# Performance work log

Measured on AMD Instinct MI355X. Metric: run time of the kernel, lower is better.

Reference implementation:

```python
import jax, jax.numpy as jnp
import numpy as np

B, P, E = 256, 196, 2048           # batch, num_pixels, encoder_size
H, A, EMB = 2048, 512, 300         # hidden, attention, embedding dims
V_IN, V_OUT = 262, 261             # input vocab (classes+2), output (classes+1)
T = 7                              # max_seq_len + 2


def setup_inputs() -> dict:
    key = jax.random.key(0)
    ks = jax.random.split(key, 20)
    s = 0.02
    return {
        "encoder_feature_out": jax.random.normal(ks[0], (B, P, E), jnp.float32),
        "encoder_out": jax.random.normal(ks[1], (B, E), jnp.float32),
        "annotations_X": jax.random.randint(ks[2], (B, T), 0, V_IN),
        "is_train": 1,
        "emb_W": jax.random.normal(ks[3], (V_IN, EMB), jnp.float32) * s,
        "feat_W": jax.random.normal(ks[4], (H, E), jnp.float32) * s,
        "feat_b": jnp.zeros((H,), jnp.float32),
        "W_ih": jax.random.normal(ks[5], (4 * H, EMB + E), jnp.float32) * s,
        "W_hh": jax.random.normal(ks[6], (4 * H, H), jnp.float32) * s,
        "b_ih": jnp.zeros((4 * H,), jnp.float32),
        "b_hh": jnp.zeros((4 * H,), jnp.float32),
        "enc_att_W": jax.random.normal(ks[7], (A, E), jnp.float32) * s,
        "enc_att_b": jnp.zeros((A,), jnp.float32),
        "dec_att_W": jax.random.normal(ks[8], (A, H), jnp.float32) * s,
        "dec_att_b": jnp.zeros((A,), jnp.float32),
        "full_att_W": jax.random.normal(ks[9], (1, A), jnp.float32) * s,
        "full_att_b": jnp.zeros((1,), jnp.float32),
        "fbeta_W": jax.random.normal(ks[10], (E, H), jnp.float32) * s,
        "fbeta_b": jnp.zeros((E,), jnp.float32),
        "fc_W": jax.random.normal(ks[11], (V_OUT, H), jnp.float32) * s,
        "fc_b": jnp.zeros((V_OUT,), jnp.float32),
    }


def _forward(encoder_feature_out, encoder_out, annotations_X,
             emb_W, feat_W, feat_b, W_ih, W_hh, b_ih, b_hh,
             enc_att_W, enc_att_b, dec_att_W, dec_att_b,
             full_att_W, full_att_b, fbeta_W, fbeta_b, fc_W, fc_b):
    enc = encoder_feature_out                                  # (B,P,E)
    # encoder side of additive attention is constant across steps
    att1 = jnp.einsum('bpe,ae->bpa', enc, enc_att_W) + enc_att_b  # (B,P,A)
    h0 = encoder_out @ feat_W.T + feat_b                       # (B,H)
    c0 = jnp.zeros_like(h0)

    def step(carry, ann_t):
        h, c = carry
        # additive attention
        att2 = h @ dec_att_W.T + dec_att_b                     # (B,A)
        e = jax.nn.relu(att1 + att2[:, None, :]) @ full_att_W[0] + full_att_b[0]  # (B,P)
        alpha = jax.nn.softmax(e, axis=1)                      # (B,P)
        awe = jnp.einsum('bp,bpe->be', alpha, enc)             # (B,E)
        gate = jax.nn.sigmoid(h @ fbeta_W.T + fbeta_b)         # (B,E)
        awe = gate * awe
        # LSTMCell (dropout layers in eval mode -> identity)
        x = jnp.concatenate([emb_W[ann_t], awe], axis=1)       # (B,EMB+E)
        gates = x @ W_ih.T + b_ih + h @ W_hh.T + b_hh          # (B,4H)
        i, f, g, o = jnp.split(gates, 4, axis=1)
        c = jax.nn.sigmoid(f) * c + jax.nn.sigmoid(i) * jnp.tanh(g)
        h = jax.nn.sigmoid(o) * jnp.tanh(c)
        yhat = h @ fc_W.T + fc_b                               # (B,V_OUT)
        return (h, c), (yhat, alpha)

    _, (yhats, alphas) = jax.lax.scan(step, (h0, c0), annotations_X.T)  # (T,B,...)
    return jnp.transpose(yhats, (1, 0, 2)), jnp.transpose(alphas, (1, 0, 2))


def reference(encoder_feature_out, encoder_out, annotations_X, is_train,
              emb_W, feat_W, feat_b, W_ih, W_hh, b_ih, b_hh,
              enc_att_W, enc_att_b, dec_att_W, dec_att_b,
              full_att_W, full_att_b, fbeta_W, fbeta_b, fc_W, fc_b):
    # is_train=True (teacher forcing) path
    return _forward(encoder_feature_out, encoder_out, annotations_X,
                    emb_W, feat_W, feat_b, W_ih, W_hh, b_ih, b_hh,
                    enc_att_W, enc_att_b, dec_att_W, dec_att_b,
                    full_att_W, full_att_b, fbeta_W, fbeta_b, fc_W, fc_b)
```

## Files before the change

### kernel.cpp

```cpp
#include <hip/hip_runtime.h>
#include <math.h>

#define B_    256
#define P_    196
#define E_    2048
#define H_    2048
#define A_    512
#define EMB_  300
#define VOUT_ 261
#define T_    7

#define KPAD_   4480
#define EMBOFF_ 2048
#define AWEOFF_ 2352

#define NSTEP_  2880
#define FCOFF_  2560

typedef __attribute__((ext_vector_type(8))) short          short8_t;
typedef __attribute__((ext_vector_type(8))) unsigned short ushort8_t;
typedef __attribute__((ext_vector_type(4))) float          f32x4;

__device__ __forceinline__ unsigned short f2b(float f) {
    union { float f; unsigned int u; } v; v.f = f;
    unsigned int x = v.u;
    unsigned int r = (x + 0x7fffu + ((x >> 16) & 1u)) >> 16;
    return (unsigned short)r;
}
__device__ __forceinline__ float b2f(unsigned short u) {
    union { unsigned int u; float f; } v; v.u = ((unsigned int)u) << 16;
    return v.f;
}

template<bool SPLITK, bool OUT16>
__global__ __launch_bounds__(256)
void gemm_sk(const unsigned short* __restrict__ Ab, int lda,
             const unsigned short* __restrict__ Bw, int ldb,
             void* __restrict__ Cout, int ldc,
             int Kper, int colbase, const float* __restrict__ bias)
{
    __shared__ ushort8_t As8[256 * 8];
    __shared__ ushort8_t Bs8[64 * 8];

    const int tid  = threadIdx.x;
    const int lane = tid & 63;
    const int w    = tid >> 6;
    const int col0 = colbase + blockIdx.x * 64;
    const int kbase = SPLITK ? blockIdx.y * Kper : 0;
    const int mrow0 = SPLITK ? 0 : blockIdx.y * 256;

    const int rb  = tid >> 3;
    const int seg = tid & 7;
    const int swz = seg ^ (rb & 7);

    const unsigned short* Ap = Ab + (size_t)(mrow0 + rb) * lda + kbase + seg * 8;
    const unsigned short* Bp = Bw + (size_t)(col0 + rb) * ldb + kbase + seg * 8;

    const int lr = lane & 15;
    const int hi = lane >> 4;

    f32x4 acc[4][4];
    #pragma unroll
    for (int m = 0; m < 4; ++m)
        #pragma unroll
        for (int n = 0; n < 4; ++n)
            acc[m][n] = (f32x4){0.f, 0.f, 0.f, 0.f};

    ushort8_t aR[8], bR[2];
    #pragma unroll
    for (int i = 0; i < 8; ++i)
        aR[i] = *(const ushort8_t*)(Ap + (size_t)i * 32 * lda);
    bR[0] = *(const ushort8_t*)(Bp);
    bR[1] = *(const ushort8_t*)(Bp + (size_t)32 * ldb);

    for (int k0 = 0; k0 < Kper; k0 += 64) {
        __syncthreads();
        #pragma unroll
        for (int i = 0; i < 8; ++i)
            As8[(rb + i * 32) * 8 + swz] = aR[i];
        Bs8[rb * 8 + swz]        = bR[0];
        Bs8[(rb + 32) * 8 + swz] = bR[1];
        __syncthreads();
        if (k0 + 64 < Kper) {
            #pragma unroll
            for (int i = 0; i < 8; ++i)
                aR[i] = *(const ushort8_t*)(Ap + (size_t)i * 32 * lda + k0 + 64);
            bR[0] = *(const ushort8_t*)(Bp + k0 + 64);
            bR[1] = *(const ushort8_t*)(Bp + (size_t)32 * ldb + k0 + 64);
        }
        #pragma unroll
        for (int kc = 0; kc < 2; ++kc) {
            short8_t af[4], bf[4];
            #pragma unroll
            for (int m = 0; m < 4; ++m) {
                const int row = w * 64 + m * 16 + lr;
                af[m] = *(const short8_t*)&As8[row * 8 + ((kc * 4 + hi) ^ (row & 7))];
            }
            #pragma unroll
            for (int n = 0; n < 4; ++n) {
                const int row = n * 16 + lr;
                bf[n] = *(const short8_t*)&Bs8[row * 8 + ((kc * 4 + hi) ^ (row & 7))];
            }
            #pragma unroll
            for (int m = 0; m < 4; ++m)
                #pragma unroll
                for (int n = 0; n < 4; ++n)
                    acc[m][n] = __builtin_amdgcn_mfma_f32_16x16x32_bf16(
                        af[m], bf[n], acc[m][n], 0, 0, 0);
        }
    }

    if (OUT16) {
        unsigned short* C16 = (unsigned short*)Cout;
        #pragma unroll
        for (int m = 0; m < 4; ++m) {
            const int grow0 = mrow0 + w * 64 + m * 16 + hi * 4;
            #pragma unroll
            for (int n = 0; n < 4; ++n) {
                const int gcol = col0 + n * 16 + lr;
                const float bv = bias[gcol];
                #pragma unroll
                for (int r = 0; r < 4; ++r)
                    C16[(size_t)(grow0 + r) * ldc + gcol] = f2b(acc[m][n][r] + bv);
            }
        }
    } else {
        float* Cs = (float*)Cout + (SPLITK ? (size_t)blockIdx.y * 256 * ldc : 0);
        #pragma unroll
        for (int m = 0; m < 4; ++m) {
            const int grow0 = w * 64 + m * 16 + hi * 4;
            #pragma unroll
            for (int n = 0; n < 4; ++n) {
                const int gcol = col0 + n * 16 + lr;
                #pragma unroll
                for (int r = 0; r < 4; ++r)
                    Cs[(size_t)(grow0 + r) * ldc + gcol] = acc[m][n][r];
            }
        }
    }
}

template<bool ABF16>
__global__ __launch_bounds__(256)
void gemm_mfma(const void* __restrict__ Ap, int lda,
               const unsigned short* __restrict__ Bw, int ldb,
               unsigned short* __restrict__ Cp, int ldc,
               const float* __restrict__ bias,
               int M, int N, int K)
{
    __shared__ __align__(16) unsigned short As[64][40];
    __shared__ __align__(16) unsigned short Bs[128][40];

    const int tid  = threadIdx.x;
    const int lane = tid & 63;
    const int wid  = tid >> 6;
    const int wr   = wid >> 1;
    const int wc   = wid & 1;
    const int row0 = blockIdx.y * 64;
    const int col0 = blockIdx.x * 128;

    const int ar = tid >> 2;
    const int as = (tid & 3) * 8;
    const int br = tid >> 1;
    const int bs = (tid & 1) * 16;

    const int lr = lane & 15;
    const int lk = (lane >> 4) * 8;

    f32x4 acc[2][4];
    #pragma unroll
    for (int m = 0; m < 2; ++m)
        #pragma unroll
        for (int n = 0; n < 4; ++n)
            acc[m][n] = (f32x4){0.f, 0.f, 0.f, 0.f};

    for (int k0 = 0; k0 < K; k0 += 32) {
        ushort8_t aval = {0,0,0,0,0,0,0,0};
        if (row0 + ar < M) {
            if (ABF16) {
                const unsigned short* A16 = (const unsigned short*)Ap;
                aval = *(const ushort8_t*)(A16 + (size_t)(row0 + ar) * lda + k0 + as);
            } else {
                const float* Af = (const float*)Ap;
                const float* p = Af + (size_t)(row0 + ar) * lda + k0 + as;
                float4 v0 = *(const float4*)(p);
                float4 v1 = *(const float4*)(p + 4);
                aval[0] = f2b(v0.x); aval[1] = f2b(v0.y);
                aval[2] = f2b(v0.z); aval[3] = f2b(v0.w);
                aval[4] = f2b(v1.x); aval[5] = f2b(v1.y);
                aval[6] = f2b(v1.z); aval[7] = f2b(v1.w);
            }
        }
        ushort8_t bv0 = {0,0,0,0,0,0,0,0}, bv1 = {0,0,0,0,0,0,0,0};
        if (col0 + br < N) {
            const unsigned short* p = Bw + (size_t)(col0 + br) * ldb + k0 + bs;
            bv0 = *(const ushort8_t*)(p);
            bv1 = *(const ushort8_t*)(p + 8);
        }
        __syncthreads();
        *(ushort8_t*)&As[ar][as]     = aval;
        *(ushort8_t*)&Bs[br][bs]     = bv0;
        *(ushort8_t*)&Bs[br][bs + 8] = bv1;
        __syncthreads();

        short8_t af[2], bf[4];
        #pragma unroll
        for (int m = 0; m < 2; ++m)
            af[m] = *(const short8_t*)&As[wr * 32 + m * 16 + lr][lk];
        #pragma unroll
        for (int n = 0; n < 4; ++n)
            bf[n] = *(const short8_t*)&Bs[wc * 64 + n * 16 + lr][lk];
        #pragma unroll
        for (int m = 0; m < 2; ++m)
            #pragma unroll
            for (int n = 0; n < 4; ++n)
                acc[m][n] = __builtin_amdgcn_mfma_f32_16x16x32_bf16(
                    af[m], bf[n], acc[m][n], 0, 0, 0);
    }

    #pragma unroll
    for (int m = 0; m < 2; ++m) {
        const int grow0 = row0 + wr * 32 + m * 16 + (lane >> 4) * 4;
        #pragma unroll
        for (int n = 0; n < 4; ++n) {
            const int gcol = col0 + wc * 64 + n * 16 + lr;
            if (gcol >= N) continue;
            const float bv = bias[gcol];
            #pragma unroll
            for (int r = 0; r < 4; ++r) {
                const int grow = grow0 + r;
                if (grow >= M) continue;
                Cp[(size_t)grow * ldc + gcol] = f2b(acc[m][n][r] + bv);
            }
        }
    }
}

__global__ __launch_bounds__(256)
void cvt_bf16_kernel(const float* __restrict__ in, unsigned short* __restrict__ out,
                     int n8)
{
    const int idx = blockIdx.x * 256 + threadIdx.x;
    if (idx >= n8) return;
    const size_t base = (size_t)idx * 8;
    float4 v0 = *(const float4*)(in + base);
    float4 v1 = *(const float4*)(in + base + 4);
    ushort8_t u;
    u[0]=f2b(v0.x); u[1]=f2b(v0.y); u[2]=f2b(v0.z); u[3]=f2b(v0.w);
    u[4]=f2b(v1.x); u[5]=f2b(v1.y); u[6]=f2b(v1.z); u[7]=f2b(v1.w);
    *(ushort8_t*)(out + base) = u;
}

__global__ __launch_bounds__(256)
void build_wcat_kernel(const float* __restrict__ W_ih, const float* __restrict__ W_hh,
                       unsigned short* __restrict__ wcat)
{
    const int row = blockIdx.x;
    const int LIH = EMB_ + E_;
    for (int s = threadIdx.x; s < KPAD_ / 8; s += 256) {
        const int k0 = s * 8;
        ushort8_t u;
        const float* src = nullptr;
        if (k0 + 8 <= H_)                        src = W_hh + (size_t)row * H_ + k0;
        else if (k0 >= H_ && k0 + 8 <= 2344)     src = W_ih + (size_t)row * LIH + (k0 - H_);
        else if (k0 >= AWEOFF_ && k0 + 8 <= 4400) src = W_ih + (size_t)row * LIH + (k0 - 2052);
        if (src) {
            float4 v0 = *(const float4*)(src);
            float4 v1 = *(const float4*)(src + 4);
            u[0]=f2b(v0.x); u[1]=f2b(v0.y); u[2]=f2b(v0.z); u[3]=f2b(v0.w);
            u[4]=f2b(v1.x); u[5]=f2b(v1.y); u[6]=f2b(v1.z); u[7]=f2b(v1.w);
        } else {
            #pragma unroll
            for (int i = 0; i < 8; ++i) {
                const int k = k0 + i;
                float v = 0.f;
                if (k >= H_ && k < 2348)              v = W_ih[(size_t)row * LIH + (k - H_)];
                else if (k >= AWEOFF_ && k < 4400)    v = W_ih[(size_t)row * LIH + (k - 2052)];
                u[i] = f2b(v);
            }
        }
        *(ushort8_t*)(wcat + (size_t)row * KPAD_ + k0) = u;
    }
}

__global__ __launch_bounds__(256)
void build_wstep_kernel(const float* __restrict__ dec_attW,
                        const float* __restrict__ fbeta_W,
                        const float* __restrict__ fc_W,
                        unsigned short* __restrict__ wstep)
{
    const int row = blockIdx.x;
    const int c0  = threadIdx.x * 8;
    const float* src;
    if (row < A_)                   src = dec_attW + (size_t)row * H_ + c0;
    else if (row < A_ + E_)         src = fbeta_W + (size_t)(row - A_) * H_ + c0;
    else if (row < A_ + E_ + VOUT_) src = fc_W + (size_t)(row - A_ - E_) * H_ + c0;
    else                            src = nullptr;
    ushort8_t u = {0,0,0,0,0,0,0,0};
    if (src) {
        float4 v0 = *(const float4*)(src);
        float4 v1 = *(const float4*)(src + 4);
        u[0]=f2b(v0.x); u[1]=f2b(v0.y); u[2]=f2b(v0.z); u[3]=f2b(v0.w);
        u[4]=f2b(v1.x); u[5]=f2b(v1.y); u[6]=f2b(v1.z); u[7]=f2b(v1.w);
    }
    *(ushort8_t*)(wstep + (size_t)row * H_ + c0) = u;
}

__global__ __launch_bounds__(256)
void reduce_h0(const float* __restrict__ parts, const float* __restrict__ bias,
               unsigned short* __restrict__ xcat)
{
    const int i = blockIdx.x * 256 + threadIdx.x;
    const int row = i >> 11, col = i & (H_ - 1);
    float acc = bias[col];
    #pragma unroll
    for (int s = 0; s < 8; ++s)
        acc += parts[(size_t)s * 256 * H_ + i];
    xcat[(size_t)row * KPAD_ + col] = f2b(acc);
}

__global__ __launch_bounds__(256)
void fused_att(const float* __restrict__ parts, const float* __restrict__ dec_attb,
               const unsigned short* __restrict__ att1,
               const float* __restrict__ fw_g, const float* __restrict__ fb,
               float* __restrict__ alpha, float* __restrict__ out_a, int t)
{
    const int b = blockIdx.x;
    const int tid = threadIdx.x;
    const int lane = tid & 63;
    const int wid  = tid >> 6;
    __shared__ float att2s[A_];
    __shared__ float es[P_];
    __shared__ float red[4];

    #pragma unroll
    for (int it = 0; it < A_ / 256; ++it) {
        const int c = tid + it * 256;
        float acc = dec_attb[c];
        #pragma unroll
        for (int s = 0; s < 8; ++s)
            acc += parts[((size_t)s * B_ + b) * NSTEP_ + c];
        att2s[c] = acc;
    }
    __syncthreads();

    float a2r[8], fwr[8];
    #pragma unroll
    for (int k = 0; k < 8; ++k) {
        a2r[k] = att2s[lane * 8 + k];
        fwr[k] = fw_g[lane * 8 + k];
    }
    const float fbv = fb[0];

    for (int p = wid; p < P_; p += 4) {
        ushort8_t v = *(const ushort8_t*)(att1 + ((size_t)b * P_ + p) * A_ + lane * 8);
        float acc = 0.f;
        #pragma unroll
        for (int k = 0; k < 8; ++k) {
            float x = b2f(v[k]) + a2r[k];
            x = x > 0.f ? x : 0.f;
            acc = fmaf(x, fwr[k], acc);
        }
        #pragma unroll
        for (int off = 32; off > 0; off >>= 1)
            acc += __shfl_xor(acc, off);
        if (lane == 0) es[p] = acc + fbv;
    }
    __syncthreads();

    float v = (tid < P_) ? es[tid] : -1e30f;
    float m = v;
    #pragma unroll
    for (int off = 32; off > 0; off >>= 1)
        m = fmaxf(m, __shfl_xor(m, off));
    if (lane == 0) red[wid] = m;
    __syncthreads();
    m = fmaxf(fmaxf(red[0], red[1]), fmaxf(red[2], red[3]));
    __syncthreads();
    float p = (tid < P_) ? expf(v - m) : 0.f;
    float s = p;
    #pragma unroll
    for (int off = 32; off > 0; off >>= 1)
        s += __shfl_xor(s, off);
    if (lane == 0) red[wid] = s;
    __syncthreads();
    s = red[0] + red[1] + red[2] + red[3];
    if (tid < P_) {
        const float a = p / s;
        alpha[b * P_ + tid] = a;
        out_a[((size_t)b * T_ + t) * P_ + tid] = a;
    }
}

__global__ __launch_bounds__(256)
void fused_awe(const float* __restrict__ parts, const float* __restrict__ fbeta_b,
               const float* __restrict__ alpha,
               const float* __restrict__ encf, const unsigned short* __restrict__ enc16,
               int use16,
               const int* __restrict__ ann, const float* __restrict__ embW,
               unsigned short* __restrict__ xcat, int t)
{
    const int b = blockIdx.x;
    const int tid = threadIdx.x;
    __shared__ float al[P_];
    if (tid < P_) al[tid] = alpha[b * P_ + tid];
    __syncthreads();

    const int e0 = tid * 8;
    float g[8];
    #pragma unroll
    for (int k = 0; k < 8; ++k) {
        float acc = fbeta_b[e0 + k];
        #pragma unroll
        for (int s = 0; s < 8; ++s)
            acc += parts[((size_t)s * B_ + b) * NSTEP_ + A_ + e0 + k];
        g[k] = 1.f / (1.f + expf(-acc));
    }

    float acc[8] = {0.f,0.f,0.f,0.f,0.f,0.f,0.f,0.f};
    if (use16) {
        const unsigned short* ep = enc16 + (size_t)b * P_ * E_ + e0;
        for (int p = 0; p < P_; p += 2) {
            ushort8_t v0 = *(const ushort8_t*)(ep + (size_t)p * E_);
            ushort8_t v1 = *(const ushort8_t*)(ep + (size_t)(p + 1) * E_);
            const float a0 = al[p], a1 = al[p + 1];
            #pragma unroll
            for (int k = 0; k < 8; ++k)
                acc[k] = fmaf(a1, b2f(v1[k]), fmaf(a0, b2f(v0[k]), acc[k]));
        }
    } else {
        const float* ep = encf + (size_t)b * P_ * E_ + e0;
        for (int p = 0; p < P_; ++p) {
            float4 v0 = *(const float4*)(ep + (size_t)p * E_);
            float4 v1 = *(const float4*)(ep + (size_t)p * E_ + 4);
            const float a0 = al[p];
            acc[0] = fmaf(a0, v0.x, acc[0]); acc[1] = fmaf(a0, v0.y, acc[1]);
            acc[2] = fmaf(a0, v0.z, acc[2]); acc[3] = fmaf(a0, v0.w, acc[3]);
            acc[4] = fmaf(a0, v1.x, acc[4]); acc[5] = fmaf(a0, v1.y, acc[5]);
            acc[6] = fmaf(a0, v1.z, acc[6]); acc[7] = fmaf(a0, v1.w, acc[7]);
        }
    }
    ushort8_t o;
    #pragma unroll
    for (int k = 0; k < 8; ++k) o[k] = f2b(g[k] * acc[k]);
    *(ushort8_t*)(xcat + (size_t)b * KPAD_ + AWEOFF_ + e0) = o;

    const int r = ann[b * T_ + t];
    for (int j = tid; j < EMB_; j += 256)
        xcat[(size_t)b * KPAD_ + EMBOFF_ + j] = f2b(embW[(size_t)r * EMB_ + j]);
}

__global__ __launch_bounds__(256)
void fc_reduce(const float* __restrict__ parts, const float* __restrict__ fc_b,
               float* __restrict__ out_y, int tm1)
{
    const int i = blockIdx.x * 256 + threadIdx.x;
    if (i >= B_ * VOUT_) return;
    const int b = i / VOUT_;
    const int c = i - b * VOUT_;
    float acc = fc_b[c];
    #pragma unroll
    for (int s = 0; s < 8; ++s)
        acc += parts[((size_t)s * B_ + b) * NSTEP_ + FCOFF_ + c];
    out_y[((size_t)b * T_ + tm1) * VOUT_ + c] = acc;
}

__global__ __launch_bounds__(256)
void lstm_kernel(const float* __restrict__ parts, const float* __restrict__ bias4h,
                 float* __restrict__ c, unsigned short* __restrict__ xcat)
{
    const int idx = blockIdx.x * 256 + threadIdx.x;
    const int b = idx >> 11;
    const int j = idx & (H_ - 1);
    const float* p0 = parts + (size_t)b * 4 * H_;
    const float* p1 = p0 + (size_t)256 * 4 * H_;
    const float gi = bias4h[j]          + p0[j]          + p1[j];
    const float gf = bias4h[H_ + j]     + p0[H_ + j]     + p1[H_ + j];
    const float gg = bias4h[2 * H_ + j] + p0[2 * H_ + j] + p1[2 * H_ + j];
    const float go = bias4h[3 * H_ + j] + p0[3 * H_ + j] + p1[3 * H_ + j];
    const float si = 1.f / (1.f + expf(-gi));
    const float sf = 1.f / (1.f + expf(-gf));
    const float so = 1.f / (1.f + expf(-go));
    const float cn = sf * c[idx] + si * tanhf(gg);
    c[idx] = cn;
    xcat[(size_t)b * KPAD_ + j] = f2b(so * tanhf(cn));
}

__global__ __launch_bounds__(256)
void addvec_kernel(const float* __restrict__ a, const float* __restrict__ b,
                   float* __restrict__ o, int n)
{
    const int i = blockIdx.x * 256 + threadIdx.x;
    if (i < n) o[i] = a[i] + b[i];
}

extern "C" void kernel_launch(void* const* d_in, const int* in_sizes, int n_in,
                              void* d_out, int out_size, void* d_ws, size_t ws_size,
                              hipStream_t stream)
{
    const float* enc      = (const float*)d_in[0];
    const float* enc_out  = (const float*)d_in[1];
    const int*   ann      = (const int*)  d_in[2];
    const float* emb_W    = (const float*)d_in[4];
    const float* feat_W   = (const float*)d_in[5];
    const float* feat_b   = (const float*)d_in[6];
    const float* W_ih     = (const float*)d_in[7];
    const float* W_hh     = (const float*)d_in[8];
    const float* b_ih     = (const float*)d_in[9];
    const float* b_hh     = (const float*)d_in[10];
    const float* enc_attW = (const float*)d_in[11];
    const float* enc_attb = (const float*)d_in[12];
    const float* dec_attW = (const float*)d_in[13];
    const float* dec_attb = (const float*)d_in[14];
    const float* full_attW= (const float*)d_in[15];
    const float* full_attb= (const float*)d_in[16];
    const float* fbeta_W  = (const float*)d_in[17];
    const float* fbeta_b  = (const float*)d_in[18];
    const float* fc_W     = (const float*)d_in[19];
    const float* fc_b     = (const float*)d_in[20];
    (void)in_sizes; (void)n_in; (void)out_size;

    float* out   = (float*)d_out;
    float* out_y = out;
    float* out_a = out + (size_t)B_ * T_ * VOUT_;

    char* base = (char*)d_ws;
    size_t off = 0;
    auto alloc = [&](size_t bytes) -> char* {
        char* p = base + off;
        off += (bytes + 255) & ~(size_t)255;
        return p;
    };
    unsigned short* att1_16   = (unsigned short*)alloc((size_t)B_ * P_ * A_ * 2);
    unsigned short* wcat16    = (unsigned short*)alloc((size_t)4 * H_ * KPAD_ * 2);
    unsigned short* wstep16   = (unsigned short*)alloc((size_t)NSTEP_ * H_ * 2);
    unsigned short* encattW16 = (unsigned short*)alloc((size_t)A_ * E_ * 2);
    unsigned short* featW16   = (unsigned short*)alloc((size_t)H_ * E_ * 2);
    unsigned short* encout16  = (unsigned short*)alloc((size_t)B_ * E_ * 2);
    unsigned short* xcat16    = (unsigned short*)alloc((size_t)B_ * KPAD_ * 2);
    float* cbuf    = (float*)alloc((size_t)B_ * H_ * 4);
    float* alpha   = (float*)alloc((size_t)B_ * P_ * 4);
    float* bias4h  = (float*)alloc((size_t)4 * H_ * 4);
    float* parts   = (float*)alloc((size_t)8 * B_ * NSTEP_ * 4);
    const size_t enc_elems = (size_t)B_ * P_ * E_;
    const int use16 = (off + enc_elems * 2 <= ws_size) ? 1 : 0;
    unsigned short* enc16 = use16 ? (unsigned short*)alloc(enc_elems * 2) : nullptr;

    const dim3 blk(256);

    addvec_kernel<<<dim3((4 * H_ + 255) / 256), blk, 0, stream>>>(b_ih, b_hh, bias4h, 4 * H_);
    cvt_bf16_kernel<<<dim3((A_ * E_ / 8 + 255) / 256), blk, 0, stream>>>(enc_attW, encattW16, A_ * E_ / 8);
    cvt_bf16_kernel<<<dim3((H_ * E_ / 8 + 255) / 256), blk, 0, stream>>>(feat_W, featW16, H_ * E_ / 8);
    cvt_bf16_kernel<<<dim3((B_ * E_ / 8 + 255) / 256), blk, 0, stream>>>(enc_out, encout16, B_ * E_ / 8);
    build_wcat_kernel<<<dim3(4 * H_), blk, 0, stream>>>(W_ih, W_hh, wcat16);
    build_wstep_kernel<<<dim3(NSTEP_), blk, 0, stream>>>(dec_attW, fbeta_W, fc_W, wstep16);
    hipMemsetAsync(xcat16, 0, (size_t)B_ * KPAD_ * 2, stream);
    hipMemsetAsync(cbuf, 0, (size_t)B_ * H_ * 4, stream);
    if (use16)
        cvt_bf16_kernel<<<dim3((int)(enc_elems / 8 + 255) / 256), blk, 0, stream>>>(enc, enc16, (int)(enc_elems / 8));

    if (use16) {
        dim3 g(A_ / 64, (B_ * P_) / 256);
        gemm_sk<false, true><<<g, blk, 0, stream>>>(enc16, E_, encattW16, E_,
            att1_16, A_, E_, 0, enc_attb);
    } else {
        dim3 g((A_ + 127) / 128, (B_ * P_) / 64);
        gemm_mfma<false><<<g, blk, 0, stream>>>(enc, E_, encattW16, E_,
            att1_16, A_, enc_attb, B_ * P_, A_, E_);
    }
    gemm_sk<true, false><<<dim3(H_ / 64, 8), blk, 0, stream>>>(encout16, E_, featW16, E_,
        parts, H_, E_ / 8, 0, nullptr);
    reduce_h0<<<dim3(B_ * H_ / 256), blk, 0, stream>>>(parts, feat_b, xcat16);

    for (int t = 0; t <= T_; ++t) {
        if (t < T_)
            gemm_sk<true, false><<<dim3(NSTEP_ / 64, 8), blk, 0, stream>>>(
                xcat16, KPAD_, wstep16, H_, parts, NSTEP_, H_ / 8, 0, nullptr);
        else
            gemm_sk<true, false><<<dim3((NSTEP_ - FCOFF_) / 64, 8), blk, 0, stream>>>(
                xcat16, KPAD_, wstep16, H_, parts, NSTEP_, H_ / 8, FCOFF_, nullptr);
        if (t > 0)
            fc_reduce<<<dim3((B_ * VOUT_ + 255) / 256), blk, 0, stream>>>(parts, fc_b, out_y, t - 1);
        if (t == T_) break;

        fused_att<<<dim3(B_), blk, 0, stream>>>(parts, dec_attb, att1_16,
                                                full_attW, full_attb, alpha, out_a, t);
        fused_awe<<<dim3(B_), blk, 0, stream>>>(parts, fbeta_b, alpha, enc, enc16,
                                                use16, ann, emb_W, xcat16, t);

        gemm_sk<true, false><<<dim3(4 * H_ / 64, 2), blk, 0, stream>>>(
            xcat16, KPAD_, wcat16, KPAD_, parts, 4 * H_, KPAD_ / 2, 0, nullptr);
        lstm_kernel<<<dim3(B_ * H_ / 256), blk, 0, stream>>>(parts, bias4h, cbuf, xcat16);
    }
}
```

Before: 1.458 ms.

## Fuse enc bf16 conversion into att1 GEMM, XCD swizzle, 4-way gate split-K, fold fc reduce

The att1 GEMM now reads fp32 encoder features directly and converts them to bf16 in registers. The blocks with nblk==0 also write the bf16 copy, so the separate full-tensor conversion pass is gone. It uses a 1D grid with an XCD-aware block swizzle. The gate GEMM moves from 2-way to 4-way split-K, with KPAD padded to 4608, and the LSTM kernel sums 4 partials. The fc reduction for earlier steps is folded into fused_awe, and the attention and awe loops are retuned: half-warps per pixel, and 4 pixels per iteration. The trade-off is more partial-sum traffic and extra padded K work.

```diff
diff --git a/kernel.cpp b/kernel.cpp
--- a/kernel.cpp
+++ b/kernel.cpp
@@ -10,12 +10,13 @@
 #define VOUT_ 261
 #define T_    7
 
-#define KPAD_   4480
+#define KPAD_   4608
 #define EMBOFF_ 2048
 #define AWEOFF_ 2352
 
 #define NSTEP_  2880
 #define FCOFF_  2560
+#define GSPLIT_ 4
 
 typedef __attribute__((ext_vector_type(8))) short          short8_t;
 typedef __attribute__((ext_vector_type(8))) unsigned short ushort8_t;
@@ -31,13 +32,20 @@
     union { unsigned int u; float f; } v; v.u = ((unsigned int)u) << 16;
     return v.f;
 }
-
-template<bool SPLITK, bool OUT16>
-__global__ __launch_bounds__(256)
-void gemm_sk(const unsigned short* __restrict__ Ab, int lda,
+__device__ __forceinline__ ushort8_t pack8(float4 u0, float4 u1) {
+    ushort8_t u;
+    u[0]=f2b(u0.x); u[1]=f2b(u0.y); u[2]=f2b(u0.z); u[3]=f2b(u0.w);
+    u[4]=f2b(u1.x); u[5]=f2b(u1.y); u[6]=f2b(u1.z); u[7]=f2b(u1.w);
+    return u;
+}
+
+template<bool SPLITK, bool OUT16, bool XCDSWZ, bool AF32>
+__global__ __launch_bounds__(256)
+void gemm_sk(const void* __restrict__ Ab, int lda,
              const unsigned short* __restrict__ Bw, int ldb,
              void* __restrict__ Cout, int ldc,
-             int Kper, int colbase, const float* __restrict__ bias)
+             int Kper, int colbase, const float* __restrict__ bias,
+             int nbx, unsigned short* __restrict__ Aout16)
 {
     __shared__ ushort8_t As8[256 * 8];
     __shared__ ushort8_t Bs8[64 * 8];
@@ -45,15 +53,25 @@
     const int tid  = threadIdx.x;
     const int lane = tid & 63;
     const int w    = tid >> 6;
-    const int col0 = colbase + blockIdx.x * 64;
+
+    int nblk, mblk;
+    if (XCDSWZ) {
+        const int bid  = blockIdx.x;
+        const int pair = (bid & 7) * (gridDim.x >> 3) + (bid >> 3);
+        nblk = pair % nbx;
+        mblk = pair / nbx;
+    } else {
+        nblk = blockIdx.x;
+        mblk = 0;
+    }
+    const int col0  = colbase + nblk * 64;
     const int kbase = SPLITK ? blockIdx.y * Kper : 0;
-    const int mrow0 = SPLITK ? 0 : blockIdx.y * 256;
+    const int mrow0 = XCDSWZ ? mblk * 256 : 0;
 
     const int rb  = tid >> 3;
     const int seg = tid & 7;
     const int swz = seg ^ (rb & 7);
 
-    const unsigned short* Ap = Ab + (size_t)(mrow0 + rb) * lda + kbase + seg * 8;
     const unsigned short* Bp = Bw + (size_t)(col0 + rb) * ldb + kbase + seg * 8;
 
     const int lr = lane & 15;
@@ -67,9 +85,22 @@
             acc[m][n] = (f32x4){0.f, 0.f, 0.f, 0.f};
 
     ushort8_t aR[8], bR[2];
-    #pragma unroll
-    for (int i = 0; i < 8; ++i)
-        aR[i] = *(const ushort8_t*)(Ap + (size_t)i * 32 * lda);
+    const unsigned short* Ap16 = nullptr;
+    const float* Apf = nullptr;
+    if (AF32) Apf  = (const float*)Ab + (size_t)(mrow0 + rb) * lda + kbase + seg * 8;
+    else      Ap16 = (const unsigned short*)Ab + (size_t)(mrow0 + rb) * lda + kbase + seg * 8;
+    unsigned short* Aw16 = AF32 ? (Aout16 + (size_t)(mrow0 + rb) * lda + kbase + seg * 8) : nullptr;
+
+    #pragma unroll
+    for (int i = 0; i < 8; ++i) {
+        if (AF32) {
+            const float* p = Apf + (size_t)i * 32 * lda;
+            aR[i] = pack8(*(const float4*)(p), *(const float4*)(p + 4));
+            if (nblk == 0) *(ushort8_t*)(Aw16 + (size_t)i * 32 * lda) = aR[i];
+        } else {
+            aR[i] = *(const ushort8_t*)(Ap16 + (size_t)i * 32 * lda);
+        }
+    }
     bR[0] = *(const ushort8_t*)(Bp);
     bR[1] = *(const ushort8_t*)(Bp + (size_t)32 * ldb);
 
@@ -83,8 +114,16 @@
         __syncthreads();
         if (k0 + 64 < Kper) {
             #pragma unroll
-            for (int i = 0; i < 8; ++i)
-                aR[i] = *(const ushort8_t*)(Ap + (size_t)i * 32 * lda + k0 + 64);
+            for (int i = 0; i < 8; ++i) {
+                if (AF32) {
+                    const float* p = Apf + (size_t)i * 32 * lda + k0 + 64;
+                    aR[i] = pack8(*(const float4*)(p), *(const float4*)(p + 4));
+                    if (nblk == 0)
+                        *(ushort8_t*)(Aw16 + (size_t)i * 32 * lda + k0 + 64) = aR[i];
+                } else {
+                    aR[i] = *(const ushort8_t*)(Ap16 + (size_t)i * 32 * lda + k0 + 64);
+                }
+            }
             bR[0] = *(const ushort8_t*)(Bp + k0 + 64);
             bR[1] = *(const ushort8_t*)(Bp + (size_t)32 * ldb + k0 + 64);
         }
@@ -140,13 +179,12 @@
     }
 }
 
-template<bool ABF16>
-__global__ __launch_bounds__(256)
-void gemm_mfma(const void* __restrict__ Ap, int lda,
-               const unsigned short* __restrict__ Bw, int ldb,
-               unsigned short* __restrict__ Cp, int ldc,
-               const float* __restrict__ bias,
-               int M, int N, int K)
+__global__ __launch_bounds__(256)
+void gemm_mfma_f32(const float* __restrict__ Af, int lda,
+                   const unsigned short* __restrict__ Bw, int ldb,
+                   unsigned short* __restrict__ Cp, int ldc,
+                   const float* __restrict__ bias,
+                   int M, int N, int K)
 {
     __shared__ __align__(16) unsigned short As[64][40];
     __shared__ __align__(16) unsigned short Bs[128][40];
@@ -177,19 +215,8 @@
     for (int k0 = 0; k0 < K; k0 += 32) {
         ushort8_t aval = {0,0,0,0,0,0,0,0};
         if (row0 + ar < M) {
-            if (ABF16) {
-                const unsigned short* A16 = (const unsigned short*)Ap;
-                aval = *(const ushort8_t*)(A16 + (size_t)(row0 + ar) * lda + k0 + as);
-            } else {
-                const float* Af = (const float*)Ap;
-                const float* p = Af + (size_t)(row0 + ar) * lda + k0 + as;
-                float4 v0 = *(const float4*)(p);
-                float4 v1 = *(const float4*)(p + 4);
-                aval[0] = f2b(v0.x); aval[1] = f2b(v0.y);
-                aval[2] = f2b(v0.z); aval[3] = f2b(v0.w);
-                aval[4] = f2b(v1.x); aval[5] = f2b(v1.y);
-                aval[6] = f2b(v1.z); aval[7] = f2b(v1.w);
-            }
+            const float* p = Af + (size_t)(row0 + ar) * lda + k0 + as;
+            aval = pack8(*(const float4*)(p), *(const float4*)(p + 4));
         }
         ushort8_t bv0 = {0,0,0,0,0,0,0,0}, bv1 = {0,0,0,0,0,0,0,0};
         if (col0 + br < N) {
@@ -243,12 +270,8 @@
     const int idx = blockIdx.x * 256 + threadIdx.x;
     if (idx >= n8) return;
     const size_t base = (size_t)idx * 8;
-    float4 v0 = *(const float4*)(in + base);
-    float4 v1 = *(const float4*)(in + base + 4);
-    ushort8_t u;
-    u[0]=f2b(v0.x); u[1]=f2b(v0.y); u[2]=f2b(v0.z); u[3]=f2b(v0.w);
-    u[4]=f2b(v1.x); u[5]=f2b(v1.y); u[6]=f2b(v1.z); u[7]=f2b(v1.w);
-    *(ushort8_t*)(out + base) = u;
+    *(ushort8_t*)(out + base) =
+        pack8(*(const float4*)(in + base), *(const float4*)(in + base + 4));
 }
 
 __global__ __launch_bounds__(256)
@@ -261,21 +284,18 @@
         const int k0 = s * 8;
         ushort8_t u;
         const float* src = nullptr;
-        if (k0 + 8 <= H_)                        src = W_hh + (size_t)row * H_ + k0;
-        else if (k0 >= H_ && k0 + 8 <= 2344)     src = W_ih + (size_t)row * LIH + (k0 - H_);
+        if (k0 + 8 <= H_)                         src = W_hh + (size_t)row * H_ + k0;
+        else if (k0 >= H_ && k0 + 8 <= 2344)      src = W_ih + (size_t)row * LIH + (k0 - H_);
         else if (k0 >= AWEOFF_ && k0 + 8 <= 4400) src = W_ih + (size_t)row * LIH + (k0 - 2052);
         if (src) {
-            float4 v0 = *(const float4*)(src);
-            float4 v1 = *(const float4*)(src + 4);
-            u[0]=f2b(v0.x); u[1]=f2b(v0.y); u[2]=f2b(v0.z); u[3]=f2b(v0.w);
-            u[4]=f2b(v1.x); u[5]=f2b(v1.y); u[6]=f2b(v1.z); u[7]=f2b(v1.w);
+            u = pack8(*(const float4*)(src), *(const float4*)(src + 4));
         } else {
             #pragma unroll
             for (int i = 0; i < 8; ++i) {
                 const int k = k0 + i;
                 float v = 0.f;
-                if (k >= H_ && k < 2348)              v = W_ih[(size_t)row * LIH + (k - H_)];
-                else if (k >= AWEOFF_ && k < 4400)    v = W_ih[(size_t)row * LIH + (k - 2052)];
+                if (k >= H_ && k < 2348)           v = W_ih[(size_t)row * LIH + (k - H_)];
+                else if (k >= AWEOFF_ && k < 4400) v = W_ih[(size_t)row * LIH + (k - 2052)];
                 u[i] = f2b(v);
             }
         }
@@ -297,12 +317,7 @@
     else if (row < A_ + E_ + VOUT_) src = fc_W + (size_t)(row - A_ - E_) * H_ + c0;
     else                            src = nullptr;
     ushort8_t u = {0,0,0,0,0,0,0,0};
-    if (src) {
-        float4 v0 = *(const float4*)(src);
-        float4 v1 = *(const float4*)(src + 4);
-        u[0]=f2b(v0.x); u[1]=f2b(v0.y); u[2]=f2b(v0.z); u[3]=f2b(v0.w);
-        u[4]=f2b(v1.x); u[5]=f2b(v1.y); u[6]=f2b(v1.z); u[7]=f2b(v1.w);
-    }
+    if (src) u = pack8(*(const float4*)(src), *(const float4*)(src + 4));
     *(ushort8_t*)(wstep + (size_t)row * H_ + c0) = u;
 }
 
@@ -344,27 +359,37 @@
     }
     __syncthreads();
 
-    float a2r[8], fwr[8];
-    #pragma unroll
-    for (int k = 0; k < 8; ++k) {
-        a2r[k] = att2s[lane * 8 + k];
-        fwr[k] = fw_g[lane * 8 + k];
+    const int l32  = lane & 31;
+    const int slot = wid * 2 + (lane >> 5);
+    float a2r[16], fwr[16];
+    #pragma unroll
+    for (int k = 0; k < 16; ++k) {
+        a2r[k] = att2s[l32 * 16 + k];
+        fwr[k] = fw_g[l32 * 16 + k];
     }
     const float fbv = fb[0];
 
-    for (int p = wid; p < P_; p += 4) {
-        ushort8_t v = *(const ushort8_t*)(att1 + ((size_t)b * P_ + p) * A_ + lane * 8);
+    for (int p = slot; p < P_; p += 8) {
+        const unsigned short* row = att1 + ((size_t)b * P_ + p) * A_ + l32 * 16;
+        ushort8_t v0 = *(const ushort8_t*)(row);
+        ushort8_t v1 = *(const ushort8_t*)(row + 8);
         float acc = 0.f;
         #pragma unroll
         for (int k = 0; k < 8; ++k) {
-            float x = b2f(v[k]) + a2r[k];
+            float x = b2f(v0[k]) + a2r[k];
             x = x > 0.f ? x : 0.f;
             acc = fmaf(x, fwr[k], acc);
         }
         #pragma unroll
-        for (int off = 32; off > 0; off >>= 1)
+        for (int k = 0; k < 8; ++k) {
+            float x = b2f(v1[k]) + a2r[k + 8];
+            x = x > 0.f ? x : 0.f;
+            acc = fmaf(x, fwr[k + 8], acc);
+        }
+        #pragma unroll
+        for (int off = 16; off > 0; off >>= 1)
             acc += __shfl_xor(acc, off);
-        if (lane == 0) es[p] = acc + fbv;
+        if (l32 == 0) es[p] = acc + fbv;
     }
     __syncthreads();
 
@@ -398,7 +423,8 @@
                const float* __restrict__ encf, const unsigned short* __restrict__ enc16,
                int use16,
                const int* __restrict__ ann, const float* __restrict__ embW,
-               unsigned short* __restrict__ xcat, int t)
+               unsigned short* __restrict__ xcat,
+               const float* __restrict__ fc_b, float* __restrict__ out_y, int t)
 {
     const int b = blockIdx.x;
     const int tid = threadIdx.x;
@@ -420,13 +446,19 @@
     float acc[8] = {0.f,0.f,0.f,0.f,0.f,0.f,0.f,0.f};
     if (use16) {
         const unsigned short* ep = enc16 + (size_t)b * P_ * E_ + e0;
-        for (int p = 0; p < P_; p += 2) {
-            ushort8_t v0 = *(const ushort8_t*)(ep + (size_t)p * E_);
+        for (int p = 0; p < P_; p += 4) {
+            ushort8_t v0 = *(const ushort8_t*)(ep + (size_t)(p + 0) * E_);
             ushort8_t v1 = *(const ushort8_t*)(ep + (size_t)(p + 1) * E_);
-            const float a0 = al[p], a1 = al[p + 1];
-            #pragma unroll
-            for (int k = 0; k < 8; ++k)
-                acc[k] = fmaf(a1, b2f(v1[k]), fmaf(a0, b2f(v0[k]), acc[k]));
+            ushort8_t v2 = *(const ushort8_t*)(ep + (size_t)(p + 2) * E_);
+            ushort8_t v3 = *(const ushort8_t*)(ep + (size_t)(p + 3) * E_);
+            const float a0 = al[p], a1 = al[p + 1], a2 = al[p + 2], a3 = al[p + 3];
+            #pragma unroll
+            for (int k = 0; k < 8; ++k) {
+                float t0 = fmaf(a0, b2f(v0[k]), acc[k]);
+                float t1 = fmaf(a1, b2f(v1[k]), t0);
+                float t2 = fmaf(a2, b2f(v2[k]), t1);
+                acc[k]   = fmaf(a3, b2f(v3[k]), t2);
+            }
         }
     } else {
         const float* ep = encf + (size_t)b * P_ * E_ + e0;
@@ -448,6 +480,16 @@
     const int r = ann[b * T_ + t];
     for (int j = tid; j < EMB_; j += 256)
         xcat[(size_t)b * KPAD_ + EMBOFF_ + j] = f2b(embW[(size_t)r * EMB_ + j]);
+
+    if (t > 0) {
+        for (int c = tid; c < VOUT_; c += 256) {
+            float a = fc_b[c];
+            #pragma unroll
+            for (int s = 0; s < 8; ++s)
+                a += parts[((size_t)s * B_ + b) * NSTEP_ + FCOFF_ + c];
+            out_y[((size_t)b * T_ + (t - 1)) * VOUT_ + c] = a;
+        }
+    }
 }
 
 __global__ __launch_bounds__(256)
@@ -473,11 +515,14 @@
     const int b = idx >> 11;
     const int j = idx & (H_ - 1);
     const float* p0 = parts + (size_t)b * 4 * H_;
-    const float* p1 = p0 + (size_t)256 * 4 * H_;
-    const float gi = bias4h[j]          + p0[j]          + p1[j];
-    const float gf = bias4h[H_ + j]     + p0[H_ + j]     + p1[H_ + j];
-    const float gg = bias4h[2 * H_ + j] + p0[2 * H_ + j] + p1[2 * H_ + j];
-    const float go = bias4h[3 * H_ + j] + p0[3 * H_ + j] + p1[3 * H_ + j];
+    const size_t S = (size_t)256 * 4 * H_;
+    float gi = bias4h[j],          gf = bias4h[H_ + j];
+    float gg = bias4h[2 * H_ + j], go = bias4h[3 * H_ + j];
+    #pragma unroll
+    for (int s = 0; s < GSPLIT_; ++s) {
+        const float* p = p0 + s * S;
+        gi += p[j]; gf += p[H_ + j]; gg += p[2 * H_ + j]; go += p[3 * H_ + j];
+    }
     const float si = 1.f / (1.f + expf(-gi));
     const float sf = 1.f / (1.f + expf(-gf));
     const float so = 1.f / (1.f + expf(-go));
@@ -541,7 +586,8 @@
     float* cbuf    = (float*)alloc((size_t)B_ * H_ * 4);
     float* alpha   = (float*)alloc((size_t)B_ * P_ * 4);
     float* bias4h  = (float*)alloc((size_t)4 * H_ * 4);
-    float* parts   = (float*)alloc((size_t)8 * B_ * NSTEP_ * 4);
+    const size_t parts_elems = (size_t)GSPLIT_ * B_ * 4 * H_;
+    float* parts   = (float*)alloc(parts_elems * 4);
     const size_t enc_elems = (size_t)B_ * P_ * E_;
     const int use16 = (off + enc_elems * 2 <= ws_size) ? 1 : 0;
     unsigned short* enc16 = use16 ? (unsigned short*)alloc(enc_elems * 2) : nullptr;
@@ -556,40 +602,39 @@
     build_wstep_kernel<<<dim3(NSTEP_), blk, 0, stream>>>(dec_attW, fbeta_W, fc_W, wstep16);
     hipMemsetAsync(xcat16, 0, (size_t)B_ * KPAD_ * 2, stream);
     hipMemsetAsync(cbuf, 0, (size_t)B_ * H_ * 4, stream);
-    if (use16)
-        cvt_bf16_kernel<<<dim3((int)(enc_elems / 8 + 255) / 256), blk, 0, stream>>>(enc, enc16, (int)(enc_elems / 8));
 
     if (use16) {
-        dim3 g(A_ / 64, (B_ * P_) / 256);
-        gemm_sk<false, true><<<g, blk, 0, stream>>>(enc16, E_, encattW16, E_,
-            att1_16, A_, E_, 0, enc_attb);
+        gemm_sk<false, true, true, true><<<dim3(196 * 8), blk, 0, stream>>>(
+            enc, E_, encattW16, E_, att1_16, A_, E_, 0, enc_attb, 8, enc16);
     } else {
         dim3 g((A_ + 127) / 128, (B_ * P_) / 64);
-        gemm_mfma<false><<<g, blk, 0, stream>>>(enc, E_, encattW16, E_,
+        gemm_mfma_f32<<<g, blk, 0, stream>>>(enc, E_, encattW16, E_,
             att1_16, A_, enc_attb, B_ * P_, A_, E_);
     }
-    gemm_sk<true, false><<<dim3(H_ / 64, 8), blk, 0, stream>>>(encout16, E_, featW16, E_,
-        parts, H_, E_ / 8, 0, nullptr);
+    gemm_sk<true, false, false, false><<<dim3(H_ / 64, 8), blk, 0, stream>>>(
+        encout16, E_, featW16, E_, parts, H_, E_ / 8, 0, nullptr, 0, nullptr);
     reduce_h0<<<dim3(B_ * H_ / 256), blk, 0, stream>>>(parts, feat_b, xcat16);
 
     for (int t = 0; t <= T_; ++t) {
         if (t < T_)
-            gemm_sk<true, false><<<dim3(NSTEP_ / 64, 8), blk, 0, stream>>>(
-                xcat16, KPAD_, wstep16, H_, parts, NSTEP_, H_ / 8, 0, nullptr);
+            gemm_sk<true, false, false, false><<<dim3(NSTEP_ / 64, 8), blk, 0, stream>>>(
+                xcat16, KPAD_, wstep16, H_, parts, NSTEP_, H_ / 8, 0, nullptr, 0, nullptr);
         else
-            gemm_sk<true, false><<<dim3((NSTEP_ - FCOFF_) / 64, 8), blk, 0, stream>>>(
-                xcat16, KPAD_, wstep16, H_, parts, NSTEP_, H_ / 8, FCOFF_, nullptr);
-        if (t > 0)
+            gemm_sk<true, false, false, false><<<dim3((NSTEP_ - FCOFF_) / 64, 8), blk, 0, stream>>>(
+                xcat16, KPAD_, wstep16, H_, parts, NSTEP_, H_ / 8, FCOFF_, nullptr, 0, nullptr);
+        if (t == T_) {
             fc_reduce<<<dim3((B_ * VOUT_ + 255) / 256), blk, 0, stream>>>(parts, fc_b, out_y, t - 1);
-        if (t == T_) break;
+            break;
+        }
 
         fused_att<<<dim3(B_), blk, 0, stream>>>(parts, dec_attb, att1_16,
                                                 full_attW, full_attb, alpha, out_a, t);
         fused_awe<<<dim3(B_), blk, 0, stream>>>(parts, fbeta_b, alpha, enc, enc16,
-                                                use16, ann, emb_W, xcat16, t);
-
-        gemm_sk<true, false><<<dim3(4 * H_ / 64, 2), blk, 0, stream>>>(
-            xcat16, KPAD_, wcat16, KPAD_, parts, 4 * H_, KPAD_ / 2, 0, nullptr);
+                                                use16, ann, emb_W, xcat16,
+                                                fc_b, out_y, t);
+
+        gemm_sk<true, false, false, false><<<dim3(4 * H_ / 64, GSPLIT_), blk, 0, stream>>>(
+            xcat16, KPAD_, wcat16, KPAD_, parts, 4 * H_, KPAD_ / GSPLIT_, 0, nullptr, 0, nullptr);
         lstm_kernel<<<dim3(B_ * H_ / 256), blk, 0, stream>>>(parts, bias4h, cbuf, xcat16);
     }
 }
```

After: 1.684 ms. +15.5%, slower.
